# Kernel optimization log

Measured on AMD Instinct MI355X. Metric: run time of the kernel, lower is better.

## Reference

```python
import jax, jax.numpy as jnp
import numpy as np

DIM = 256
HEADS = 8
DIM_HEAD = 64
INNER = HEADS * DIM_HEAD
NUM_BANDS = 16          # hard-coded in __init__
MAX_FREQ = 16.0         # hard-coded in __init__
NORM_SCALE = 51.0       # hard-coded in __init__
RPE_DIM = (NUM_BANDS * 2 + 1) * 2  # 66


def fourier_encode(x, max_freq, num_bands):
    # x: [...] -> [..., 2*num_bands+1]  (sin bands, cos bands, raw)
    x = x[..., None]
    scales = jnp.linspace(1.0, max_freq / 2.0, num_bands, dtype=x.dtype)
    xs = x * scales * jnp.pi
    return jnp.concatenate([jnp.sin(xs), jnp.cos(xs), x], axis=-1)


def rpe_features(query_pos, key_pos):
    # delta[b,i,j] = key_pos[b,j] - query_pos[b,i]  -> [B,Nq,Nk,2]
    delta = key_pos[:, None, :, :] - query_pos[:, :, None, :]
    dx = delta[..., 0] / NORM_SCALE
    dy = delta[..., 1] / NORM_SCALE
    dx = dx / (1.0 + jnp.abs(dx))
    dy = dy / (1.0 + jnp.abs(dy))
    x_enc = fourier_encode(dx, MAX_FREQ, NUM_BANDS)
    y_enc = fourier_encode(dy, MAX_FREQ, NUM_BANDS)
    return jnp.concatenate([x_enc, y_enc], axis=-1)  # [B,Nq,Nk,RPE_DIM]


def setup_inputs() -> dict:
    key = jax.random.key(0)
    ks = jax.random.split(key, 8)
    B, N = 1, 512
    x = jax.random.normal(ks[0], (B, N, DIM), dtype=jnp.float32)
    positions = jax.random.uniform(ks[1], (B, N, 2), dtype=jnp.float32) * 512.0
    s = 0.02
    Wq = jax.random.normal(ks[2], (DIM, INNER), dtype=jnp.float32) * s
    Wk = jax.random.normal(ks[3], (DIM + RPE_DIM, INNER), dtype=jnp.float32) * s
    Wv = jax.random.normal(ks[4], (DIM, INNER), dtype=jnp.float32) * s
    Wo = jax.random.normal(ks[5], (INNER, DIM), dtype=jnp.float32) * s
    bo = jnp.zeros((DIM,), dtype=jnp.float32)
    return {"x": x, "positions": positions, "Wq": Wq, "Wk": Wk, "Wv": Wv, "Wo": Wo, "bo": bo}


def reference(x, positions, Wq, Wk, Wv, Wo, bo):
    B, N, D = x.shape
    H, d = HEADS, DIM_HEAD
    scale = d ** -0.5

    rpe = rpe_features(positions, positions)          # [B,N,N,R]
    q = (x @ Wq).reshape(B, N, H, d)                  # [B,N,H,d]
    v = (x @ Wv).reshape(B, N, H, d)

    # k_ij = W_k @ concat(x_j, rpe_ij); split Wk to avoid expanding x to [B,N,N,D]
    Wk_x, Wk_r = Wk[:D], Wk[D:]
    k_content = x @ Wk_x                               # [B,N,INNER] (key j part)
    k_rpe = jnp.einsum('bijr,re->bije', rpe, Wk_r)     # [B,N,N,INNER]
    k = (k_content[:, None, :, :] + k_rpe).reshape(B, N, N, H, d)

    scores = jnp.einsum('bihd,bijhd->bhij', q, k) * scale
    attn = jax.nn.softmax(scores, axis=-1)
    out = jnp.einsum('bhij,bjhd->bihd', attn, v).reshape(B, N, H * d)
    return out @ Wo + bo
```

## Files before the change

kernel.cpp:

```cpp
#include <hip/hip_runtime.h>
#include <math.h>

#define NQ      512
#define DMODEL  256
#define DINNER  512
#define NH      8
#define DHEAD   64
#define SCALE   0.125f
#define PI_F    3.14159265358979323846f

#define Q_OFF   0
#define KC_OFF  262144
#define V_OFF   524288
#define QW_OFF  786432
#define IN_OFF  1064960
#define PA_OFF  1327104
#define PM_OFF  3424256
#define PL_OFF  3457024

__global__ __launch_bounds__(256) void k_proj(
    const float* __restrict__ x, const float* __restrict__ Wq,
    const float* __restrict__ Wk, const float* __restrict__ Wv,
    float* __restrict__ ws)
{
    const int z = blockIdx.z;
    const float* W = (z == 0) ? Wq : (z == 1) ? Wk : Wv;
    float* out = ws + ((z == 0) ? Q_OFF : (z == 1) ? KC_OFF : V_OFF);

    __shared__ alignas(16) float Xs[32][68];
    __shared__ alignas(16) float Bs[32][64];

    const int tx = threadIdx.x, ty = threadIdx.y;
    const int tid = ty * 16 + tx;
    const int row0 = blockIdx.y * 64, col0 = blockIdx.x * 64;

    float acc[4][4] = {};

    for (int k0 = 0; k0 < DMODEL; k0 += 32) {
        {
            const int m = tid >> 2;
            const int kk0 = (tid & 3) * 8;
            const float* src = x + (row0 + m) * DMODEL + k0 + kk0;
            float4 a0 = *(const float4*)(src);
            float4 a1 = *(const float4*)(src + 4);
            Xs[kk0 + 0][m] = a0.x; Xs[kk0 + 1][m] = a0.y;
            Xs[kk0 + 2][m] = a0.z; Xs[kk0 + 3][m] = a0.w;
            Xs[kk0 + 4][m] = a1.x; Xs[kk0 + 5][m] = a1.y;
            Xs[kk0 + 6][m] = a1.z; Xs[kk0 + 7][m] = a1.w;
        }
        {
            const int kk = tid >> 3;
            const int n0 = (tid & 7) * 8;
            const float* src = W + (k0 + kk) * DINNER + col0 + n0;
            *(float4*)&Bs[kk][n0]     = *(const float4*)(src);
            *(float4*)&Bs[kk][n0 + 4] = *(const float4*)(src + 4);
        }
        __syncthreads();
        #pragma unroll
        for (int kk = 0; kk < 32; ++kk) {
            float4 a4 = *(const float4*)&Xs[kk][ty * 4];
            float4 b4 = *(const float4*)&Bs[kk][tx * 4];
            float a[4] = {a4.x, a4.y, a4.z, a4.w};
            float b[4] = {b4.x, b4.y, b4.z, b4.w};
            #pragma unroll
            for (int ia = 0; ia < 4; ++ia)
                #pragma unroll
                for (int ib = 0; ib < 4; ++ib)
                    acc[ia][ib] += a[ia] * b[ib];
        }
        __syncthreads();
    }
    #pragma unroll
    for (int ia = 0; ia < 4; ++ia) {
        float4 o = make_float4(acc[ia][0], acc[ia][1], acc[ia][2], acc[ia][3]);
        *(float4*)&out[(row0 + ty * 4 + ia) * DINNER + col0 + tx * 4] = o;
    }
}

__global__ __launch_bounds__(256) void k_qw(
    const float* __restrict__ Wk, float* __restrict__ ws)
{
    const float* q = ws + Q_OFF;
    float* qW = ws + QW_OFF;
    const int h  = blockIdx.x >> 4;
    const int i0 = (blockIdx.x & 15) * 32;

    __shared__ float WrT[64][67];
    __shared__ alignas(16) float Qs[32][68];
    const int tid = threadIdx.x;

    for (int idx = tid; idx < 66 * 64; idx += 256) {
        int r = idx >> 6, d = idx & 63;
        WrT[d][r] = Wk[(DMODEL + r) * DINNER + h * DHEAD + d];
    }
    for (int idx = tid; idx < 32 * 16; idx += 256) {
        int m = idx >> 4, dq = (idx & 15) * 4;
        *(float4*)&Qs[m][dq] = *(const float4*)&q[(i0 + m) * DINNER + h * DHEAD + dq];
    }
    __syncthreads();

    for (int idx = tid; idx < 32 * 66; idx += 256) {
        int m = idx / 66, r = idx - m * 66;
        float acc = 0.f;
        #pragma unroll
        for (int d0 = 0; d0 < 64; d0 += 4) {
            float4 qf = *(const float4*)&Qs[m][d0];
            acc += qf.x * WrT[d0 + 0][r] + qf.y * WrT[d0 + 1][r]
                 + qf.z * WrT[d0 + 2][r] + qf.w * WrT[d0 + 3][r];
        }
        int p = (r < 32) ? r : (r == 32) ? 64 : (r < 65) ? (r - 1) : 65;
        qW[(i0 + m) * 544 + h * 68 + p] = acc * SCALE;
    }
}

#define BAND_STEP(WSX, WCX, WSY, WCY)                              \
    r0 += sxa * (WSX); r1 += cxa * (WCX);                          \
    r2 += sya * (WSY); r3 += cya * (WCY);                          \
    {   float tt;                                                  \
        tt = Kx * sxb - sxa; sxa = sxb; sxb = tt;                  \
        tt = Kx * cxb - cxa; cxa = cxb; cxb = tt;                  \
        tt = Ky * syb - sya; sya = syb; syb = tt;                  \
        tt = Ky * cyb - cya; cya = cyb; cyb = tt; }

__global__ __launch_bounds__(256, 2) void k_attn(
    const float* __restrict__ pos, float* __restrict__ ws)
{
    const float* q  = ws + Q_OFF;
    const float* kc = ws + KC_OFF;
    const float* v  = ws + V_OFF;
    const float* qW = ws + QW_OFF;
    float* pacc = ws + PA_OFF;
    float* pm   = ws + PM_OFF;
    float* pl   = ws + PL_OFF;

    const int c  = blockIdx.x;
    const int it = blockIdx.y;
    const int h  = blockIdx.z;
    const int tid = threadIdx.x;
    const int w = tid >> 6, l = tid & 63;
    const int i = it * 64 + l;
    const int j0 = c * 64;

    __shared__ alignas(16) float Ks[64][68];
    __shared__ alignas(16) float Vs[64][68];
    __shared__ float2 posKs[64];
    __shared__ float pmL[4][64];
    __shared__ float plL[4][64];

    {
        const int jj = tid >> 2, dg = (tid & 3) * 16;
        const float* sk = kc + (j0 + jj) * DINNER + h * DHEAD + dg;
        *(float4*)&Ks[jj][dg +  0] = *(const float4*)(sk);
        *(float4*)&Ks[jj][dg +  4] = *(const float4*)(sk + 4);
        *(float4*)&Ks[jj][dg +  8] = *(const float4*)(sk + 8);
        *(float4*)&Ks[jj][dg + 12] = *(const float4*)(sk + 12);
        const float* sv = v + (j0 + jj) * DINNER + h * DHEAD + dg;
        *(float4*)&Vs[jj][dg +  0] = *(const float4*)(sv);
        *(float4*)&Vs[jj][dg +  4] = *(const float4*)(sv + 4);
        *(float4*)&Vs[jj][dg +  8] = *(const float4*)(sv + 8);
        *(float4*)&Vs[jj][dg + 12] = *(const float4*)(sv + 12);
        if (tid < 64) posKs[tid] = *(const float2*)&pos[(j0 + tid) * 2];
    }

    float4 qv[16];
    const float* qrow = q + i * DINNER + h * DHEAD;
    #pragma unroll
    for (int d4 = 0; d4 < 16; ++d4) qv[d4] = *(const float4*)(qrow + d4 * 4);
    float4 cw[17];
    const float* qwrow = qW + i * 544 + h * 68;
    #pragma unroll
    for (int p4 = 0; p4 < 17; ++p4) cw[p4] = *(const float4*)(qwrow + p4 * 4);
    const float2 pq = *(const float2*)&pos[i * 2];

    __syncthreads();

    const int jb = w * 16;
    float sreg[16];
    float M = -1e30f;

    #pragma unroll
    for (int t = 0; t < 16; ++t) {
        const int jr = jb + t;
        float s0 = 0.f, s1 = 0.f, s2 = 0.f, s3 = 0.f;
        #pragma unroll
        for (int d4 = 0; d4 < 16; ++d4) {
            float4 kv = *(const float4*)&Ks[jr][d4 * 4];
            s0 += qv[d4].x * kv.x; s1 += qv[d4].y * kv.y;
            s2 += qv[d4].z * kv.z; s3 += qv[d4].w * kv.w;
        }
        float s = (s0 + s1) + (s2 + s3);

        float2 pk = posKs[jr];
        float dxr = (pk.x - pq.x) * (1.0f / 51.0f);
        float dyr = (pk.y - pq.y) * (1.0f / 51.0f);
        float dx = __fdividef(dxr, 1.0f + fabsf(dxr));
        float dy = __fdividef(dyr, 1.0f + fabsf(dyr));
        float thx = dx * PI_F, dlx = dx * (PI_F * 7.0f / 15.0f);
        float thy = dy * PI_F, dly = dy * (PI_F * 7.0f / 15.0f);
        float sxa, cxa, sxb, cxb, sya, cya, syb, cyb;
        __sincosf(thx,       &sxa, &cxa);
        __sincosf(thx + dlx, &sxb, &cxb);
        __sincosf(thy,       &sya, &cya);
        __sincosf(thy + dly, &syb, &cyb);
        float Kx = 2.0f * (cxa * cxb + sxa * sxb);
        float Ky = 2.0f * (cya * cyb + sya * syb);
        float r0 = 0.f, r1 = 0.f, r2 = 0.f, r3 = 0.f;
        #pragma unroll
        for (int g = 0; g < 4; ++g) {
            float4 wsx = cw[g], wcx = cw[4 + g], wsy = cw[8 + g], wcy = cw[12 + g];
            BAND_STEP(wsx.x, wcx.x, wsy.x, wcy.x)
            BAND_STEP(wsx.y, wcx.y, wsy.y, wcy.y)
            BAND_STEP(wsx.z, wcx.z, wsy.z, wcy.z)
            BAND_STEP(wsx.w, wcx.w, wsy.w, wcy.w)
        }
        float rpe = (r0 + r1) + (r2 + r3) + dx * cw[16].x + dy * cw[16].y;
        float score = s * SCALE + rpe;
        sreg[t] = score;
        M = fmaxf(M, score);
    }

    float4 av[16];
    #pragma unroll
    for (int d4 = 0; d4 < 16; ++d4) av[d4] = make_float4(0.f, 0.f, 0.f, 0.f);
    float lsum = 0.f;
    #pragma unroll
    for (int t = 0; t < 16; ++t) {
        float p = __expf(sreg[t] - M);
        lsum += p;
        const int jr = jb + t;
        #pragma unroll
        for (int d4 = 0; d4 < 16; ++d4) {
            float4 vv = *(const float4*)&Vs[jr][d4 * 4];
            av[d4].x += p * vv.x; av[d4].y += p * vv.y;
            av[d4].z += p * vv.z; av[d4].w += p * vv.w;
        }
    }

    pmL[w][l] = M; plL[w][l] = lsum;
    __syncthreads();
    float m0 = pmL[0][l], m1 = pmL[1][l], m2 = pmL[2][l], m3 = pmL[3][l];
    float Mg = fmaxf(fmaxf(m0, m1), fmaxf(m2, m3));
    float e = __expf(M - Mg);
    #pragma unroll
    for (int d4 = 0; d4 < 16; ++d4) {
        av[d4].x *= e; av[d4].y *= e; av[d4].z *= e; av[d4].w *= e;
    }
    float (*Sacc)[68] = Ks;
    if (w == 0) {
        #pragma unroll
        for (int d4 = 0; d4 < 16; ++d4) *(float4*)&Sacc[l][d4 * 4] = av[d4];
    }
    __syncthreads();
    if (w == 1) {
        #pragma unroll
        for (int d4 = 0; d4 < 16; ++d4) {
            float4 sv = *(const float4*)&Sacc[l][d4 * 4];
            sv.x += av[d4].x; sv.y += av[d4].y; sv.z += av[d4].z; sv.w += av[d4].w;
            *(float4*)&Sacc[l][d4 * 4] = sv;
        }
    }
    __syncthreads();
    if (w == 2) {
        #pragma unroll
        for (int d4 = 0; d4 < 16; ++d4) {
            float4 sv = *(const float4*)&Sacc[l][d4 * 4];
            sv.x += av[d4].x; sv.y += av[d4].y; sv.z += av[d4].z; sv.w += av[d4].w;
            *(float4*)&Sacc[l][d4 * 4] = sv;
        }
    }
    __syncthreads();
    if (w == 3) {
        float Lg = plL[0][l] * __expf(m0 - Mg) + plL[1][l] * __expf(m1 - Mg)
                 + plL[2][l] * __expf(m2 - Mg) + plL[3][l] * __expf(m3 - Mg);
        float* prow = pacc + ((size_t)((h * NQ + i) * 8 + c)) * 64;
        #pragma unroll
        for (int d4 = 0; d4 < 16; ++d4) {
            float4 sv = *(const float4*)&Sacc[l][d4 * 4];
            sv.x += av[d4].x; sv.y += av[d4].y; sv.z += av[d4].z; sv.w += av[d4].w;
            *(float4*)&prow[d4 * 4] = sv;
        }
        pm[(h * NQ + i) * 8 + c] = Mg;
        pl[(h * NQ + i) * 8 + c] = Lg;
    }
}

__global__ __launch_bounds__(256) void k_merge(float* __restrict__ ws)
{
    float* inner      = ws + IN_OFF;
    const float* pacc = ws + PA_OFF;
    const float* pm   = ws + PM_OFF;
    const float* pl   = ws + PL_OFF;

    const int g = blockIdx.x * 4 + (threadIdx.x >> 6);
    const int l = threadIdx.x & 63;

    float mv[8];
    #pragma unroll
    for (int cc = 0; cc < 8; ++cc) mv[cc] = pm[g * 8 + cc];
    float Mg = mv[0];
    #pragma unroll
    for (int cc = 1; cc < 8; ++cc) Mg = fmaxf(Mg, mv[cc]);
    float L = 0.f, a = 0.f;
    #pragma unroll
    for (int cc = 0; cc < 8; ++cc) {
        float e = __expf(mv[cc] - Mg);
        L += pl[g * 8 + cc] * e;
        a += pacc[(size_t)(g * 8 + cc) * 64 + l] * e;
    }
    const int h = g >> 9, i = g & 511;
    inner[i * DINNER + h * DHEAD + l] = a / L;
}

__global__ __launch_bounds__(256) void k_out(
    const float* __restrict__ Wo, const float* __restrict__ bo,
    float* __restrict__ ws, float* __restrict__ outp)
{
    const float* inner = ws + IN_OFF;
    const int c0 = blockIdx.x * 32;
    const int i0 = blockIdx.y * 32;

    __shared__ alignas(16) float Xs[32][36];
    __shared__ alignas(16) float Bs[32][32];
    const int tx = threadIdx.x, ty = threadIdx.y;
    const int tid = ty * 16 + tx;

    float acc[2][2] = {};
    for (int k0 = 0; k0 < DINNER; k0 += 32) {
        {
            const int m = tid >> 3;
            const int kk0 = (tid & 7) * 4;
            float4 a4 = *(const float4*)&inner[(i0 + m) * DINNER + k0 + kk0];
            Xs[kk0 + 0][m] = a4.x; Xs[kk0 + 1][m] = a4.y;
            Xs[kk0 + 2][m] = a4.z; Xs[kk0 + 3][m] = a4.w;
        }
        {
            const int kk = tid >> 3;
            const int n0 = (tid & 7) * 4;
            *(float4*)&Bs[kk][n0] = *(const float4*)&Wo[(k0 + kk) * DMODEL + c0 + n0];
        }
        __syncthreads();
        #pragma unroll
        for (int kk = 0; kk < 32; ++kk) {
            float2 a2 = *(const float2*)&Xs[kk][ty * 2];
            float2 b2 = *(const float2*)&Bs[kk][tx * 2];
            acc[0][0] += a2.x * b2.x;
            acc[0][1] += a2.x * b2.y;
            acc[1][0] += a2.y * b2.x;
            acc[1][1] += a2.y * b2.y;
        }
        __syncthreads();
    }
    #pragma unroll
    for (int ia = 0; ia < 2; ++ia) {
        float2 o;
        o.x = acc[ia][0] + bo[c0 + tx * 2 + 0];
        o.y = acc[ia][1] + bo[c0 + tx * 2 + 1];
        *(float2*)&outp[(i0 + ty * 2 + ia) * DMODEL + c0 + tx * 2] = o;
    }
}

extern "C" void kernel_launch(void* const* d_in, const int* in_sizes, int n_in,
                              void* d_out, int out_size, void* d_ws, size_t ws_size,
                              hipStream_t stream)
{
    const float* x   = (const float*)d_in[0];
    const float* pos = (const float*)d_in[1];
    const float* Wq  = (const float*)d_in[2];
    const float* Wk  = (const float*)d_in[3];
    const float* Wv  = (const float*)d_in[4];
    const float* Wo  = (const float*)d_in[5];
    const float* bo  = (const float*)d_in[6];
    float* out = (float*)d_out;
    float* ws  = (float*)d_ws;

    k_proj<<<dim3(8, 8, 3), dim3(16, 16), 0, stream>>>(x, Wq, Wk, Wv, ws);
    k_qw<<<dim3(128), dim3(256), 0, stream>>>(Wk, ws);
    k_attn<<<dim3(8, 8, 8), dim3(256), 0, stream>>>(pos, ws);
    k_merge<<<dim3(1024), dim3(256), 0, stream>>>(ws);
    k_out<<<dim3(8, 16), dim3(16, 16), 0, stream>>>(Wo, bo, ws, out);
}
```

Measured before the change: 146.4 us.

## Stage Q and qW through LDS and split PV accumulation to coalesce writes

Q rows, the per-query RPE weight rows and query positions are now loaded cooperatively into shared memory with coalesced float4 loads. Previously each lane fetched its own strided row straight from global memory. The PV accumulation now rescales by the block-wide max directly and runs in two 32-column halves, which halves the accumulator register footprint. The partial accumulators are then written to global memory by all threads in a coalesced pattern. The cost is extra shared memory, which may limit occupancy, and extra barriers in the reduction loop.

```diff
diff --git a/kernel.cpp b/kernel.cpp
--- a/kernel.cpp
+++ b/kernel.cpp
@@ -138,12 +138,15 @@
     const int h  = blockIdx.z;
     const int tid = threadIdx.x;
     const int w = tid >> 6, l = tid & 63;
-    const int i = it * 64 + l;
+    const int i0t = it * 64;
     const int j0 = c * 64;
 
     __shared__ alignas(16) float Ks[64][68];
     __shared__ alignas(16) float Vs[64][68];
+    __shared__ alignas(16) float Qls[64][68];
+    __shared__ alignas(16) float qWls[64][68];
     __shared__ float2 posKs[64];
+    __shared__ float2 posQs[64];
     __shared__ float pmL[4][64];
     __shared__ float plL[4][64];
 
@@ -159,20 +162,30 @@
         *(float4*)&Vs[jj][dg +  4] = *(const float4*)(sv + 4);
         *(float4*)&Vs[jj][dg +  8] = *(const float4*)(sv + 8);
         *(float4*)&Vs[jj][dg + 12] = *(const float4*)(sv + 12);
-        if (tid < 64) posKs[tid] = *(const float2*)&pos[(j0 + tid) * 2];
-    }
+        const float* sq = q + (i0t + jj) * DINNER + h * DHEAD + dg;
+        *(float4*)&Qls[jj][dg +  0] = *(const float4*)(sq);
+        *(float4*)&Qls[jj][dg +  4] = *(const float4*)(sq + 4);
+        *(float4*)&Qls[jj][dg +  8] = *(const float4*)(sq + 8);
+        *(float4*)&Qls[jj][dg + 12] = *(const float4*)(sq + 12);
+        for (int idx = tid; idx < 64 * 17; idx += 256) {
+            int r = idx / 17, p4 = idx - r * 17;
+            *(float4*)&qWls[r][p4 * 4] =
+                *(const float4*)&qW[(i0t + r) * 544 + h * 68 + p4 * 4];
+        }
+        if (tid < 64) {
+            posKs[tid] = *(const float2*)&pos[(j0 + tid) * 2];
+            posQs[tid] = *(const float2*)&pos[(i0t + tid) * 2];
+        }
+    }
+    __syncthreads();
 
     float4 qv[16];
-    const float* qrow = q + i * DINNER + h * DHEAD;
-    #pragma unroll
-    for (int d4 = 0; d4 < 16; ++d4) qv[d4] = *(const float4*)(qrow + d4 * 4);
+    #pragma unroll
+    for (int d4 = 0; d4 < 16; ++d4) qv[d4] = *(const float4*)&Qls[l][d4 * 4];
     float4 cw[17];
-    const float* qwrow = qW + i * 544 + h * 68;
-    #pragma unroll
-    for (int p4 = 0; p4 < 17; ++p4) cw[p4] = *(const float4*)(qwrow + p4 * 4);
-    const float2 pq = *(const float2*)&pos[i * 2];
-
-    __syncthreads();
+    #pragma unroll
+    for (int p4 = 0; p4 < 17; ++p4) cw[p4] = *(const float4*)&qWls[l][p4 * 4];
+    const float2 pq = posQs[l];
 
     const int jb = w * 16;
     float sreg[16];
@@ -219,68 +232,78 @@
         M = fmaxf(M, score);
     }
 
-    float4 av[16];
-    #pragma unroll
-    for (int d4 = 0; d4 < 16; ++d4) av[d4] = make_float4(0.f, 0.f, 0.f, 0.f);
     float lsum = 0.f;
     #pragma unroll
-    for (int t = 0; t < 16; ++t) {
-        float p = __expf(sreg[t] - M);
-        lsum += p;
-        const int jr = jb + t;
-        #pragma unroll
-        for (int d4 = 0; d4 < 16; ++d4) {
-            float4 vv = *(const float4*)&Vs[jr][d4 * 4];
-            av[d4].x += p * vv.x; av[d4].y += p * vv.y;
-            av[d4].z += p * vv.z; av[d4].w += p * vv.w;
-        }
-    }
-
+    for (int t = 0; t < 16; ++t) lsum += __expf(sreg[t] - M);
     pmL[w][l] = M; plL[w][l] = lsum;
     __syncthreads();
-    float m0 = pmL[0][l], m1 = pmL[1][l], m2 = pmL[2][l], m3 = pmL[3][l];
-    float Mg = fmaxf(fmaxf(m0, m1), fmaxf(m2, m3));
-    float e = __expf(M - Mg);
-    #pragma unroll
-    for (int d4 = 0; d4 < 16; ++d4) {
-        av[d4].x *= e; av[d4].y *= e; av[d4].z *= e; av[d4].w *= e;
-    }
+    const float m0 = pmL[0][l], m1 = pmL[1][l], m2 = pmL[2][l], m3 = pmL[3][l];
+    const float Mg = fmaxf(fmaxf(m0, m1), fmaxf(m2, m3));
+
     float (*Sacc)[68] = Ks;
-    if (w == 0) {
-        #pragma unroll
-        for (int d4 = 0; d4 < 16; ++d4) *(float4*)&Sacc[l][d4 * 4] = av[d4];
-    }
-    __syncthreads();
-    if (w == 1) {
-        #pragma unroll
-        for (int d4 = 0; d4 < 16; ++d4) {
-            float4 sv = *(const float4*)&Sacc[l][d4 * 4];
-            sv.x += av[d4].x; sv.y += av[d4].y; sv.z += av[d4].z; sv.w += av[d4].w;
-            *(float4*)&Sacc[l][d4 * 4] = sv;
-        }
-    }
-    __syncthreads();
-    if (w == 2) {
-        #pragma unroll
-        for (int d4 = 0; d4 < 16; ++d4) {
-            float4 sv = *(const float4*)&Sacc[l][d4 * 4];
-            sv.x += av[d4].x; sv.y += av[d4].y; sv.z += av[d4].z; sv.w += av[d4].w;
-            *(float4*)&Sacc[l][d4 * 4] = sv;
-        }
-    }
-    __syncthreads();
-    if (w == 3) {
-        float Lg = plL[0][l] * __expf(m0 - Mg) + plL[1][l] * __expf(m1 - Mg)
-                 + plL[2][l] * __expf(m2 - Mg) + plL[3][l] * __expf(m3 - Mg);
-        float* prow = pacc + ((size_t)((h * NQ + i) * 8 + c)) * 64;
-        #pragma unroll
-        for (int d4 = 0; d4 < 16; ++d4) {
-            float4 sv = *(const float4*)&Sacc[l][d4 * 4];
-            sv.x += av[d4].x; sv.y += av[d4].y; sv.z += av[d4].z; sv.w += av[d4].w;
-            *(float4*)&prow[d4 * 4] = sv;
-        }
-        pm[(h * NQ + i) * 8 + c] = Mg;
-        pl[(h * NQ + i) * 8 + c] = Lg;
+    #pragma unroll
+    for (int h2 = 0; h2 < 2; ++h2) {
+        float4 av[8];
+        #pragma unroll
+        for (int d4 = 0; d4 < 8; ++d4) av[d4] = make_float4(0.f, 0.f, 0.f, 0.f);
+        #pragma unroll
+        for (int t = 0; t < 16; ++t) {
+            float p = __expf(sreg[t] - Mg);
+            const int jr = jb + t;
+            #pragma unroll
+            for (int d4 = 0; d4 < 8; ++d4) {
+                float4 vv = *(const float4*)&Vs[jr][(h2 * 8 + d4) * 4];
+                av[d4].x += p * vv.x; av[d4].y += p * vv.y;
+                av[d4].z += p * vv.z; av[d4].w += p * vv.w;
+            }
+        }
+        if (w == 0) {
+            #pragma unroll
+            for (int d4 = 0; d4 < 8; ++d4)
+                *(float4*)&Sacc[l][(h2 * 8 + d4) * 4] = av[d4];
+        }
+        __syncthreads();
+        if (w == 1) {
+            #pragma unroll
+            for (int d4 = 0; d4 < 8; ++d4) {
+                float4 sv = *(const float4*)&Sacc[l][(h2 * 8 + d4) * 4];
+                sv.x += av[d4].x; sv.y += av[d4].y; sv.z += av[d4].z; sv.w += av[d4].w;
+                *(float4*)&Sacc[l][(h2 * 8 + d4) * 4] = sv;
+            }
+        }
+        __syncthreads();
+        if (w == 2) {
+            #pragma unroll
+            for (int d4 = 0; d4 < 8; ++d4) {
+                float4 sv = *(const float4*)&Sacc[l][(h2 * 8 + d4) * 4];
+                sv.x += av[d4].x; sv.y += av[d4].y; sv.z += av[d4].z; sv.w += av[d4].w;
+                *(float4*)&Sacc[l][(h2 * 8 + d4) * 4] = sv;
+            }
+        }
+        __syncthreads();
+        if (w == 3) {
+            #pragma unroll
+            for (int d4 = 0; d4 < 8; ++d4) {
+                float4 sv = *(const float4*)&Sacc[l][(h2 * 8 + d4) * 4];
+                sv.x += av[d4].x; sv.y += av[d4].y; sv.z += av[d4].z; sv.w += av[d4].w;
+                *(float4*)&Sacc[l][(h2 * 8 + d4) * 4] = sv;
+            }
+        }
+        __syncthreads();
+        for (int idx = tid; idx < 64 * 8; idx += 256) {
+            int r = idx >> 3, p4 = idx & 7;
+            *(float4*)&pacc[((size_t)((h * NQ + i0t + r) * 8 + c)) * 64 + h2 * 32 + p4 * 4] =
+                *(const float4*)&Sacc[r][(h2 * 8 + p4) * 4];
+        }
+    }
+
+    if (tid < 64) {
+        float Lg = plL[0][tid] * __expf(pmL[0][tid] - Mg)
+                 + plL[1][tid] * __expf(pmL[1][tid] - Mg)
+                 + plL[2][tid] * __expf(pmL[2][tid] - Mg)
+                 + plL[3][tid] * __expf(pmL[3][tid] - Mg);
+        pm[(h * NQ + i0t + tid) * 8 + c] = Mg;
+        pl[(h * NQ + i0t + tid) * 8 + c] = Lg;
     }
 }
 
```

Measured after the change: 180.7 us. 1.23x slower.

## Precompute content QK scores in a separate tiled kernel before attention

Applied to the files above, without the earlier changes.

Adds a k_content kernel that computes the scaled Q·K content scores per head as a register-tiled 64x64 GEMM and stores them in a new 8x512x512 workspace buffer. k_attn then reads the precomputed score instead of holding a 64-float query vector in registers and staging K tiles in shared memory. The K shared tile is dropped, and the partial-sum reduction now reuses the V tile. The aim is to lower register and LDS pressure in the RPE-heavy attention kernel and move the dot products into a more efficient GEMM. The cost is an extra launch plus writing and reading an 8 MB score buffer.

```diff
diff --git a/kernel.cpp b/kernel.cpp
--- a/kernel.cpp
+++ b/kernel.cpp
@@ -17,6 +17,7 @@
 #define PA_OFF  1327104
 #define PM_OFF  3424256
 #define PL_OFF  3457024
+#define SC_OFF  3489792
 
 __global__ __launch_bounds__(256) void k_proj(
     const float* __restrict__ x, const float* __restrict__ Wq,
@@ -113,6 +114,51 @@
     }
 }
 
+__global__ __launch_bounds__(256) void k_content(float* __restrict__ ws)
+{
+    const float* q  = ws + Q_OFF;
+    const float* kc = ws + KC_OFF;
+    float* sc = ws + SC_OFF;
+    const int h = blockIdx.z;
+    const int i0 = blockIdx.x * 64, j0 = blockIdx.y * 64;
+
+    __shared__ alignas(16) float Qt[64][68];
+    __shared__ alignas(16) float Kt[64][68];
+    const int tx = threadIdx.x, ty = threadIdx.y;
+    const int tid = ty * 16 + tx;
+    {
+        const int m = tid >> 2;
+        const int d0 = (tid & 3) * 16;
+        const float* qs = q  + (i0 + m) * DINNER + h * DHEAD + d0;
+        const float* ks = kc + (j0 + m) * DINNER + h * DHEAD + d0;
+        #pragma unroll
+        for (int l = 0; l < 16; ++l) {
+            Qt[d0 + l][m] = qs[l];
+            Kt[d0 + l][m] = ks[l];
+        }
+    }
+    __syncthreads();
+    float acc[4][4] = {};
+    #pragma unroll 8
+    for (int d = 0; d < 64; ++d) {
+        float4 a4 = *(const float4*)&Kt[d][ty * 4];
+        float4 b4 = *(const float4*)&Qt[d][tx * 4];
+        float a[4] = {a4.x, a4.y, a4.z, a4.w};
+        float b[4] = {b4.x, b4.y, b4.z, b4.w};
+        #pragma unroll
+        for (int ja = 0; ja < 4; ++ja)
+            #pragma unroll
+            for (int ib = 0; ib < 4; ++ib)
+                acc[ja][ib] += a[ja] * b[ib];
+    }
+    #pragma unroll
+    for (int ja = 0; ja < 4; ++ja) {
+        float4 o = make_float4(acc[ja][0] * SCALE, acc[ja][1] * SCALE,
+                               acc[ja][2] * SCALE, acc[ja][3] * SCALE);
+        *(float4*)&sc[((h * NQ) + j0 + ty * 4 + ja) * NQ + i0 + tx * 4] = o;
+    }
+}
+
 #define BAND_STEP(WSX, WCX, WSY, WCY)                              \
     r0 += sxa * (WSX); r1 += cxa * (WCX);                          \
     r2 += sya * (WSY); r3 += cya * (WCY);                          \
@@ -125,10 +171,9 @@
 __global__ __launch_bounds__(256, 2) void k_attn(
     const float* __restrict__ pos, float* __restrict__ ws)
 {
-    const float* q  = ws + Q_OFF;
-    const float* kc = ws + KC_OFF;
     const float* v  = ws + V_OFF;
     const float* qW = ws + QW_OFF;
+    const float* sc = ws + SC_OFF;
     float* pacc = ws + PA_OFF;
     float* pm   = ws + PM_OFF;
     float* pl   = ws + PL_OFF;
@@ -141,7 +186,6 @@
     const int i = it * 64 + l;
     const int j0 = c * 64;
 
-    __shared__ alignas(16) float Ks[64][68];
     __shared__ alignas(16) float Vs[64][68];
     __shared__ float2 posKs[64];
     __shared__ float pmL[4][64];
@@ -149,11 +193,6 @@
 
     {
         const int jj = tid >> 2, dg = (tid & 3) * 16;
-        const float* sk = kc + (j0 + jj) * DINNER + h * DHEAD + dg;
-        *(float4*)&Ks[jj][dg +  0] = *(const float4*)(sk);
-        *(float4*)&Ks[jj][dg +  4] = *(const float4*)(sk + 4);
-        *(float4*)&Ks[jj][dg +  8] = *(const float4*)(sk + 8);
-        *(float4*)&Ks[jj][dg + 12] = *(const float4*)(sk + 12);
         const float* sv = v + (j0 + jj) * DINNER + h * DHEAD + dg;
         *(float4*)&Vs[jj][dg +  0] = *(const float4*)(sv);
         *(float4*)&Vs[jj][dg +  4] = *(const float4*)(sv + 4);
@@ -161,63 +200,53 @@
         *(float4*)&Vs[jj][dg + 12] = *(const float4*)(sv + 12);
         if (tid < 64) posKs[tid] = *(const float2*)&pos[(j0 + tid) * 2];
     }
-
-    float4 qv[16];
-    const float* qrow = q + i * DINNER + h * DHEAD;
-    #pragma unroll
-    for (int d4 = 0; d4 < 16; ++d4) qv[d4] = *(const float4*)(qrow + d4 * 4);
-    float4 cw[17];
-    const float* qwrow = qW + i * 544 + h * 68;
-    #pragma unroll
-    for (int p4 = 0; p4 < 17; ++p4) cw[p4] = *(const float4*)(qwrow + p4 * 4);
-    const float2 pq = *(const float2*)&pos[i * 2];
-
     __syncthreads();
 
     const int jb = w * 16;
     float sreg[16];
     float M = -1e30f;
 
-    #pragma unroll
-    for (int t = 0; t < 16; ++t) {
-        const int jr = jb + t;
-        float s0 = 0.f, s1 = 0.f, s2 = 0.f, s3 = 0.f;
-        #pragma unroll
-        for (int d4 = 0; d4 < 16; ++d4) {
-            float4 kv = *(const float4*)&Ks[jr][d4 * 4];
-            s0 += qv[d4].x * kv.x; s1 += qv[d4].y * kv.y;
-            s2 += qv[d4].z * kv.z; s3 += qv[d4].w * kv.w;
-        }
-        float s = (s0 + s1) + (s2 + s3);
-
-        float2 pk = posKs[jr];
-        float dxr = (pk.x - pq.x) * (1.0f / 51.0f);
-        float dyr = (pk.y - pq.y) * (1.0f / 51.0f);
-        float dx = __fdividef(dxr, 1.0f + fabsf(dxr));
-        float dy = __fdividef(dyr, 1.0f + fabsf(dyr));
-        float thx = dx * PI_F, dlx = dx * (PI_F * 7.0f / 15.0f);
-        float thy = dy * PI_F, dly = dy * (PI_F * 7.0f / 15.0f);
-        float sxa, cxa, sxb, cxb, sya, cya, syb, cyb;
-        __sincosf(thx,       &sxa, &cxa);
-        __sincosf(thx + dlx, &sxb, &cxb);
-        __sincosf(thy,       &sya, &cya);
-        __sincosf(thy + dly, &syb, &cyb);
-        float Kx = 2.0f * (cxa * cxb + sxa * sxb);
-        float Ky = 2.0f * (cya * cyb + sya * syb);
-        float r0 = 0.f, r1 = 0.f, r2 = 0.f, r3 = 0.f;
-        #pragma unroll
-        for (int g = 0; g < 4; ++g) {
-            float4 wsx = cw[g], wcx = cw[4 + g], wsy = cw[8 + g], wcy = cw[12 + g];
-            BAND_STEP(wsx.x, wcx.x, wsy.x, wcy.x)
-            BAND_STEP(wsx.y, wcx.y, wsy.y, wcy.y)
-            BAND_STEP(wsx.z, wcx.z, wsy.z, wcy.z)
-            BAND_STEP(wsx.w, wcx.w, wsy.w, wcy.w)
-        }
-        float rpe = (r0 + r1) + (r2 + r3) + dx * cw[16].x + dy * cw[16].y;
-        float score = s * SCALE + rpe;
-        sreg[t] = score;
-        M = fmaxf(M, score);
-    }
+    {
+        float4 cw[17];
+        const float* qwrow = qW + i * 544 + h * 68;
+        #pragma unroll
+        for (int p4 = 0; p4 < 17; ++p4) cw[p4] = *(const float4*)(qwrow + p4 * 4);
+        const float2 pq = *(const float2*)&pos[i * 2];
+
+        #pragma unroll
+        for (int t = 0; t < 16; ++t) {
+            const int jr = jb + t;
+            const float scv = sc[((h * NQ) + j0 + jr) * NQ + i];
+            float2 pk = posKs[jr];
+            float dxr = (pk.x - pq.x) * (1.0f / 51.0f);
+            float dyr = (pk.y - pq.y) * (1.0f / 51.0f);
+            float dx = __fdividef(dxr, 1.0f + fabsf(dxr));
+            float dy = __fdividef(dyr, 1.0f + fabsf(dyr));
+            float thx = dx * PI_F, dlx = dx * (PI_F * 7.0f / 15.0f);
+            float thy = dy * PI_F, dly = dy * (PI_F * 7.0f / 15.0f);
+            float sxa, cxa, sxb, cxb, sya, cya, syb, cyb;
+            __sincosf(thx,       &sxa, &cxa);
+            __sincosf(thx + dlx, &sxb, &cxb);
+            __sincosf(thy,       &sya, &cya);
+            __sincosf(thy + dly, &syb, &cyb);
+            float Kx = 2.0f * (cxa * cxb + sxa * sxb);
+            float Ky = 2.0f * (cya * cyb + sya * syb);
+            float r0 = 0.f, r1 = 0.f, r2 = 0.f, r3 = 0.f;
+            #pragma unroll
+            for (int g = 0; g < 4; ++g) {
+                float4 wsx = cw[g], wcx = cw[4 + g], wsy = cw[8 + g], wcy = cw[12 + g];
+                BAND_STEP(wsx.x, wcx.x, wsy.x, wcy.x)
+                BAND_STEP(wsx.y, wcx.y, wsy.y, wcy.y)
+                BAND_STEP(wsx.z, wcx.z, wsy.z, wcy.z)
+                BAND_STEP(wsx.w, wcx.w, wsy.w, wcy.w)
+            }
+            float rpe = (r0 + r1) + (r2 + r3) + dx * cw[16].x + dy * cw[16].y;
+            float score = scv + rpe;
+            sreg[t] = score;
+            M = fmaxf(M, score);
+        }
+    }
+    __builtin_amdgcn_sched_barrier(0);
 
     float4 av[16];
     #pragma unroll
@@ -245,7 +274,7 @@
     for (int d4 = 0; d4 < 16; ++d4) {
         av[d4].x *= e; av[d4].y *= e; av[d4].z *= e; av[d4].w *= e;
     }
-    float (*Sacc)[68] = Ks;
+    float (*Sacc)[68] = Vs;
     if (w == 0) {
         #pragma unroll
         for (int d4 = 0; d4 < 16; ++d4) *(float4*)&Sacc[l][d4 * 4] = av[d4];
@@ -375,6 +404,7 @@
 
     k_proj<<<dim3(8, 8, 3), dim3(16, 16), 0, stream>>>(x, Wq, Wk, Wv, ws);
     k_qw<<<dim3(128), dim3(256), 0, stream>>>(Wk, ws);
+    k_content<<<dim3(8, 8, 8), dim3(16, 16), 0, stream>>>(ws);
     k_attn<<<dim3(8, 8, 8), dim3(256), 0, stream>>>(pos, ws);
     k_merge<<<dim3(1024), dim3(256), 0, stream>>>(ws);
     k_out<<<dim3(8, 16), dim3(16, 16), 0, stream>>>(Wo, bo, ws, out);
```

After: 154.5 us. 5.5% more time.
